# Performance work log

Hardware: AMD Instinct MI355X
Metric: run time of the kernel (lower is better)

The kernel has to match this reference:

```python
import jax, jax.numpy as jnp
import numpy as np

CENTER_VARIANCE = 0.1
SIZE_VARIANCE = 0.2
IOU_THRESHOLD = 0.5
EPS = 1e-5

B, G, P = 128, 64, 8732


def setup_inputs() -> dict:
    key = jax.random.key(0)
    k1, k2, k3, k4, k5 = jax.random.split(key, 5)
    # valid corner-form gt boxes in [0,1]: x2>x1, y2>y1
    xy1 = jax.random.uniform(k1, (B, G, 2)) * 0.7
    wh = jax.random.uniform(k2, (B, G, 2)) * 0.29 + 0.01
    gt_boxes = jnp.concatenate([xy1, xy1 + wh], axis=-1).astype(jnp.float32)
    gt_labels = jax.random.randint(k3, (B, G), 1, 21, dtype=jnp.int64)
    # center-form priors (cx, cy, w, h), w/h bounded away from 0
    pc = jax.random.uniform(k4, (P, 2)) * 0.9 + 0.05
    pwh = jax.random.uniform(k5, (P, 2)) * 0.9 + 0.02
    priors_center = jnp.concatenate([pc, pwh], axis=-1).astype(jnp.float32)
    return {"gt_boxes": gt_boxes, "gt_labels": gt_labels, "priors_center": priors_center}


def center_to_corner(b):
    return jnp.concatenate([b[..., :2] - b[..., 2:] / 2, b[..., :2] + b[..., 2:] / 2], axis=-1)


def corner_to_center(b):
    return jnp.concatenate([(b[..., :2] + b[..., 2:]) / 2, b[..., 2:] - b[..., :2]], axis=-1)


def area_of(lt, rb):
    hw = jnp.clip(rb - lt, 0.0, None)
    return hw[..., 0] * hw[..., 1]


def iou_of(boxes0, boxes1):
    lt = jnp.maximum(boxes0[..., :2], boxes1[..., :2])
    rb = jnp.minimum(boxes0[..., 2:], boxes1[..., 2:])
    overlap = area_of(lt, rb)
    a0 = area_of(boxes0[..., :2], boxes0[..., 2:])
    a1 = area_of(boxes1[..., :2], boxes1[..., 2:])
    return overlap / (a0 + a1 - overlap + EPS)


def _assign_one(gt_b, gt_l, corner_priors):
    # ious: [P, G]
    ious = iou_of(gt_b[None, :, :], corner_priors[:, None, :])
    best_target_per_prior = ious.max(axis=1)            # [P]
    best_target_idx = ious.argmax(axis=1)               # [P]
    best_prior_per_target_idx = ious.argmax(axis=0)     # [G]
    # force-assign each gt its best prior
    best_target_idx = best_target_idx.at[best_prior_per_target_idx].set(jnp.arange(gt_b.shape[0]))
    best_target_per_prior = best_target_per_prior.at[best_prior_per_target_idx].set(2.0)
    labels = gt_l[best_target_idx]
    labels = jnp.where(best_target_per_prior < IOU_THRESHOLD, 0, labels)
    boxes = gt_b[best_target_idx]                        # [P, 4] corner form
    return boxes, labels


def reference(gt_boxes, gt_labels, priors_center):
    corner_priors = center_to_corner(priors_center)      # [P, 4]
    boxes, labels = jax.vmap(_assign_one, in_axes=(0, 0, None))(gt_boxes, gt_labels, corner_priors)
    cb = corner_to_center(boxes)                         # [B, P, 4] center form
    loc_xy = (cb[..., :2] - priors_center[..., :2]) / (priors_center[..., 2:] * CENTER_VARIANCE)
    loc_wh = jnp.log(cb[..., 2:] / priors_center[..., 2:]) / SIZE_VARIANCE
    locations = jnp.concatenate([loc_xy, loc_wh], axis=-1)
    return locations, labels
```

## Files before the change

### kernel.cpp

```cpp
#include <hip/hip_runtime.h>

typedef float f2 __attribute__((ext_vector_type(2)));

static constexpr int B = 128;
static constexpr int G = 64;
static constexpr int P = 8732;
static constexpr float EPS = 1e-5f;
static constexpr float IOU_THR = 0.5f;

__device__ __forceinline__ void encode_store(
    float* out_loc, float* out_lab, int b, int p,
    float4 gb, float4 pr, int lab)
{
    float cx = (gb.x + gb.z) * 0.5f;
    float cy = (gb.y + gb.w) * 0.5f;
    float w  = gb.z - gb.x;
    float h  = gb.w - gb.y;
    float4 loc;
    loc.x = (cx - pr.x) / (pr.z * 0.1f);
    loc.y = (cy - pr.y) / (pr.w * 0.1f);
    loc.z = logf(w / pr.z) / 0.2f;
    loc.w = logf(h / pr.w) / 0.2f;
    *(float4*)(out_loc + (size_t)(b * P + p) * 4) = loc;
    out_lab[(size_t)b * P + p] = (float)lab;
}

__global__ __launch_bounds__(256, 8) void k_fused(
    const float* __restrict__ gt_boxes,
    const int*   __restrict__ gt_labels,
    const float* __restrict__ priors,
    unsigned long long* __restrict__ packed,
    float* __restrict__ out_loc,
    float* __restrict__ out_lab)
{
    __shared__ float s_pk[5][G];
    __shared__ unsigned long long s_red[G];
    __shared__ int   s_lab[G];
    __shared__ float s_iou[256][17];

    const int b = blockIdx.y;
    const int t = threadIdx.x;
    const int pbase = blockIdx.x * 256;
    const int p = pbase + t;
    const bool valid = p < P;

    if (t < G) {
        float4 gb = *(const float4*)(gt_boxes + (size_t)(b * G + t) * 4);
        s_pk[0][t] = gb.x; s_pk[1][t] = gb.y;
        s_pk[2][t] = gb.z; s_pk[3][t] = gb.w;
        s_pk[4][t] = __fmul_rn(fmaxf(__fsub_rn(gb.z, gb.x), 0.0f),
                               fmaxf(__fsub_rn(gb.w, gb.y), 0.0f));
        s_lab[t] = gt_labels[b * G + t];
        s_red[t] = 0ull;
    }
    __syncthreads();

    float4 pr = make_float4(0.f, 0.f, 0.f, 0.f);
    if (valid) pr = *(const float4*)(priors + (size_t)p * 4);
    float hw = __fmul_rn(pr.z, 0.5f), hh = __fmul_rn(pr.w, 0.5f);
    float px1 = __fsub_rn(pr.x, hw), py1 = __fsub_rn(pr.y, hh);
    float px2 = __fadd_rn(pr.x, hw), py2 = __fadd_rn(pr.y, hh);
    float pa  = __fmul_rn(fmaxf(__fsub_rn(px2, px1), 0.0f),
                          fmaxf(__fsub_rn(py2, py1), 0.0f));

    const f2 vpx1 = {px1, px1}, vpy1 = {py1, py1};
    const f2 vpx2 = {px2, px2}, vpy2 = {py2, py2};
    const f2 vpa  = {pa, pa},   veps = {EPS, EPS};
    const f2 vone = {1.0f, 1.0f}, vnegone = {-1.0f, -1.0f};
    const f2 vzero = {0.0f, 0.0f};

    float bestIou = -1.0f;
    int   bestG   = 0;

    for (int q = 0; q < 4; ++q) {
        const int gbase = q * 16;
#pragma unroll
        for (int k2 = 0; k2 < 8; ++k2) {
            const int g0 = gbase + 2 * k2;
            f2 gx1 = *(const f2*)&s_pk[0][g0];
            f2 gy1 = *(const f2*)&s_pk[1][g0];
            f2 gx2 = *(const f2*)&s_pk[2][g0];
            f2 gy2 = *(const f2*)&s_pk[3][g0];
            f2 ga  = *(const f2*)&s_pk[4][g0];

            f2 ltx = __builtin_elementwise_max(gx1, vpx1);
            f2 lty = __builtin_elementwise_max(gy1, vpy1);
            f2 rbx = __builtin_elementwise_min(gx2, vpx2);
            f2 rby = __builtin_elementwise_min(gy2, vpy2);
            f2 dx  = rbx - ltx;
            f2 dy  = rby - lty;
            f2 ow  = __builtin_elementwise_max(dx, vzero);
            f2 oh  = __builtin_elementwise_max(dy, vzero);
            f2 ov  = ow * oh;
            f2 t1  = ga + vpa;
            f2 t2  = __builtin_elementwise_fma(ov, vnegone, t1);
            f2 den = t2 + veps;
            f2 r0  = {__builtin_amdgcn_rcpf(den.x), __builtin_amdgcn_rcpf(den.y)};
            f2 e   = __builtin_elementwise_fma(-den, r0, vone);
            f2 r1  = __builtin_elementwise_fma(e, r0, r0);
            f2 q0  = ov * r1;
            f2 rem = __builtin_elementwise_fma(-den, q0, ov);
            f2 qq  = __builtin_elementwise_fma(rem, r1, q0);

            s_iou[t][2 * k2]     = qq.x;
            s_iou[t][2 * k2 + 1] = qq.y;
            if (qq.x > bestIou) { bestIou = qq.x; bestG = g0; }
            if (qq.y > bestIou) { bestIou = qq.y; bestG = g0 + 1; }
        }
        __syncthreads();

        {
            const int c  = t & 15;
            const int r0s = (t >> 4) * 16;
            float bv = -0.5f;
            int   br = 0;
#pragma unroll
            for (int j = 0; j < 16; ++j) {
                float v = s_iou[r0s + j][c];
                if (v > bv) { bv = v; br = r0s + j; }
            }
            unsigned long long key =
                ((unsigned long long)__float_as_uint(bv) << 32) |
                (unsigned long long)(0xFFFFFFFFu - (unsigned)(pbase + br));
            atomicMax(&s_red[gbase + c], key);
        }
        __syncthreads();
    }

    if (t < G) {
        atomicMax(&packed[(size_t)b * G + t], s_red[t]);
    }

    if (valid) {
        float4 gb = make_float4(s_pk[0][bestG], s_pk[1][bestG],
                                s_pk[2][bestG], s_pk[3][bestG]);
        int lab = (bestIou < IOU_THR) ? 0 : s_lab[bestG];
        encode_store(out_loc, out_lab, b, p, gb, pr, lab);
    }
}

__global__ __launch_bounds__(64) void k_fixup(
    const float* __restrict__ gt_boxes,
    const int*   __restrict__ gt_labels,
    const float* __restrict__ priors,
    const unsigned long long* __restrict__ packed,
    float* __restrict__ out_loc,
    float* __restrict__ out_lab)
{
    __shared__ int s_p[G];
    const int b = blockIdx.x;
    const int g = threadIdx.x;

    unsigned long long key = packed[(size_t)b * G + g];
    int p = (int)(0xFFFFFFFFu - (unsigned)(key & 0xFFFFFFFFull));
    s_p[g] = p;
    __syncthreads();

    bool win = true;
    for (int g2 = g + 1; g2 < G; ++g2)
        if (s_p[g2] == p) { win = false; break; }

    if (win) {
        float4 gb = *(const float4*)(gt_boxes + (size_t)(b * G + g) * 4);
        float4 pr = *(const float4*)(priors + (size_t)p * 4);
        int lab = gt_labels[b * G + g];
        encode_store(out_loc, out_lab, b, p, gb, pr, lab);
    }
}

extern "C" void kernel_launch(void* const* d_in, const int* in_sizes, int n_in,
                              void* d_out, int out_size, void* d_ws, size_t ws_size,
                              hipStream_t stream)
{
    const float* gt_boxes  = (const float*)d_in[0];
    const int*   gt_labels = (const int*)d_in[1];
    const float* priors    = (const float*)d_in[2];

    float* out_loc = (float*)d_out;
    float* out_lab = out_loc + (size_t)B * P * 4;
    unsigned long long* packed = (unsigned long long*)d_ws;

    hipMemsetAsync(packed, 0, (size_t)B * G * sizeof(unsigned long long), stream);

    k_fused<<<dim3((P + 255) / 256, B), 256, 0, stream>>>(
        gt_boxes, gt_labels, priors, packed, out_loc, out_lab);

    k_fixup<<<dim3(B), 64, 0, stream>>>(
        gt_boxes, gt_labels, priors, packed, out_loc, out_lab);
}
```

Before: 72.45 us.

## Precompute GT SoA with areas in prep kernel and read via uniform global loads

Adds a prep kernel that writes ground-truth boxes in structure-of-arrays form with precomputed areas to workspace and zeroes the packed reduction buffer, replacing the memset. The IoU loop now reads GT coordinates from global memory with block-uniform addresses, which can become scalar loads, instead of LDS reads. The per-prior argmax update is also restructured to compare the pair maximum once. This adds a kernel launch and depends on scalar or cached global loads being cheaper than LDS broadcasts.

```diff
diff --git a/kernel.cpp b/kernel.cpp
--- a/kernel.cpp
+++ b/kernel.cpp
@@ -25,15 +25,35 @@
     out_lab[(size_t)b * P + p] = (float)lab;
 }
 
+__global__ __launch_bounds__(64) void k_prep(
+    const float* __restrict__ gt_boxes,
+    float* __restrict__ gt_ext,
+    unsigned long long* __restrict__ packed)
+{
+    const int b = blockIdx.x;
+    const int g = threadIdx.x;
+    float4 gb = *(const float4*)(gt_boxes + (size_t)(b * G + g) * 4);
+    float ga = __fmul_rn(fmaxf(__fsub_rn(gb.z, gb.x), 0.0f),
+                         fmaxf(__fsub_rn(gb.w, gb.y), 0.0f));
+    float* ge = gt_ext + (size_t)b * 5 * G;
+    ge[0 * G + g] = gb.x;
+    ge[1 * G + g] = gb.y;
+    ge[2 * G + g] = gb.z;
+    ge[3 * G + g] = gb.w;
+    ge[4 * G + g] = ga;
+    packed[b * G + g] = 0ull;
+}
+
 __global__ __launch_bounds__(256, 8) void k_fused(
     const float* __restrict__ gt_boxes,
     const int*   __restrict__ gt_labels,
     const float* __restrict__ priors,
+    const float* __restrict__ gt_ext,
     unsigned long long* __restrict__ packed,
     float* __restrict__ out_loc,
     float* __restrict__ out_lab)
 {
-    __shared__ float s_pk[5][G];
+    __shared__ float4 s_gt[G];
     __shared__ unsigned long long s_red[G];
     __shared__ int   s_lab[G];
     __shared__ float s_iou[256][17];
@@ -44,12 +64,10 @@
     const int p = pbase + t;
     const bool valid = p < P;
 
+    const float* __restrict__ ge = gt_ext + (size_t)b * 5 * G;
+
     if (t < G) {
-        float4 gb = *(const float4*)(gt_boxes + (size_t)(b * G + t) * 4);
-        s_pk[0][t] = gb.x; s_pk[1][t] = gb.y;
-        s_pk[2][t] = gb.z; s_pk[3][t] = gb.w;
-        s_pk[4][t] = __fmul_rn(fmaxf(__fsub_rn(gb.z, gb.x), 0.0f),
-                               fmaxf(__fsub_rn(gb.w, gb.y), 0.0f));
+        s_gt[t]  = *(const float4*)(gt_boxes + (size_t)(b * G + t) * 4);
         s_lab[t] = gt_labels[b * G + t];
         s_red[t] = 0ull;
     }
@@ -72,16 +90,16 @@
     float bestIou = -1.0f;
     int   bestG   = 0;
 
-    for (int q = 0; q < 4; ++q) {
-        const int gbase = q * 16;
+    for (int q4 = 0; q4 < 4; ++q4) {
+        const int gbase = q4 * 16;
 #pragma unroll
         for (int k2 = 0; k2 < 8; ++k2) {
             const int g0 = gbase + 2 * k2;
-            f2 gx1 = *(const f2*)&s_pk[0][g0];
-            f2 gy1 = *(const f2*)&s_pk[1][g0];
-            f2 gx2 = *(const f2*)&s_pk[2][g0];
-            f2 gy2 = *(const f2*)&s_pk[3][g0];
-            f2 ga  = *(const f2*)&s_pk[4][g0];
+            f2 gx1 = *(const f2*)(ge + 0 * G + g0);
+            f2 gy1 = *(const f2*)(ge + 1 * G + g0);
+            f2 gx2 = *(const f2*)(ge + 2 * G + g0);
+            f2 gy2 = *(const f2*)(ge + 3 * G + g0);
+            f2 ga  = *(const f2*)(ge + 4 * G + g0);
 
             f2 ltx = __builtin_elementwise_max(gx1, vpx1);
             f2 lty = __builtin_elementwise_max(gy1, vpy1);
@@ -104,13 +122,15 @@
 
             s_iou[t][2 * k2]     = qq.x;
             s_iou[t][2 * k2 + 1] = qq.y;
-            if (qq.x > bestIou) { bestIou = qq.x; bestG = g0; }
-            if (qq.y > bestIou) { bestIou = qq.y; bestG = g0 + 1; }
+
+            int   selg = (qq.y > qq.x) ? g0 + 1 : g0;
+            float v    = fmaxf(qq.x, qq.y);
+            if (v > bestIou) { bestIou = v; bestG = selg; }
         }
         __syncthreads();
 
         {
-            const int c  = t & 15;
+            const int c   = t & 15;
             const int r0s = (t >> 4) * 16;
             float bv = -0.5f;
             int   br = 0;
@@ -132,10 +152,8 @@
     }
 
     if (valid) {
-        float4 gb = make_float4(s_pk[0][bestG], s_pk[1][bestG],
-                                s_pk[2][bestG], s_pk[3][bestG]);
         int lab = (bestIou < IOU_THR) ? 0 : s_lab[bestG];
-        encode_store(out_loc, out_lab, b, p, gb, pr, lab);
+        encode_store(out_loc, out_lab, b, p, s_gt[bestG], pr, lab);
     }
 }
 
@@ -178,12 +196,14 @@
 
     float* out_loc = (float*)d_out;
     float* out_lab = out_loc + (size_t)B * P * 4;
+
     unsigned long long* packed = (unsigned long long*)d_ws;
-
-    hipMemsetAsync(packed, 0, (size_t)B * G * sizeof(unsigned long long), stream);
+    float* gt_ext = (float*)((char*)d_ws + (size_t)B * G * sizeof(unsigned long long));
+
+    k_prep<<<dim3(B), 64, 0, stream>>>(gt_boxes, gt_ext, packed);
 
     k_fused<<<dim3((P + 255) / 256, B), 256, 0, stream>>>(
-        gt_boxes, gt_labels, priors, packed, out_loc, out_lab);
+        gt_boxes, gt_labels, priors, gt_ext, packed, out_loc, out_lab);
 
     k_fixup<<<dim3(B), 64, 0, stream>>>(
         gt_boxes, gt_labels, priors, packed, out_loc, out_lab);
```

New measurement: 87.81 us. 21.2% more time.
